# Kernel optimization log

Hardware: AMD Instinct MI355X
Metric: run time of the kernel (lower is better)

## Reference

```python
import jax, jax.numpy as jnp
import numpy as np

HEADS = 16

def setup_inputs() -> dict:
    key = jax.random.key(0)
    k1, k2, k3 = jax.random.split(key, 3)
    B, T, C = 4, 2048, 1024
    s = 0.02
    return {
        "x": jax.random.normal(k1, (B, T, C), dtype=jnp.float32),
        "W_qkv": jax.random.normal(k2, (C, 3 * C), dtype=jnp.float32) * s,
        "b_qkv": jnp.zeros((3 * C,), dtype=jnp.float32),
        "W_pr": jax.random.normal(k3, (C, C), dtype=jnp.float32) * s,
        "b_pr": jnp.zeros((C,), dtype=jnp.float32),
    }

def reference(x, W_qkv, b_qkv, W_pr, b_pr):
    B, T, C = x.shape
    H = HEADS
    hd = C // H
    qkv = x @ W_qkv + b_qkv                     # [B,T,3C]
    q, k, v = jnp.split(qkv, 3, axis=-1)
    # [B,T,C] -> [B,H,T,hd]
    q = q.reshape(B, T, H, hd).transpose(0, 2, 1, 3)
    k = k.reshape(B, T, H, hd).transpose(0, 2, 1, 3)
    v = v.reshape(B, T, H, hd).transpose(0, 2, 1, 3)
    att = jnp.einsum('bhqd,bhkd->bhqk', q, k) * (1.0 / jnp.sqrt(jnp.float32(hd)))
    causal = jnp.tril(jnp.ones((T, T), dtype=bool))
    att = jnp.where(causal[None, None, :, :], att, jnp.float32(-jnp.inf))
    att = jax.nn.softmax(att, axis=-1)
    y = jnp.einsum('bhqk,bhkd->bhqd', att, v)   # [B,H,T,hd]
    y = y.transpose(0, 2, 1, 3).reshape(B, T, C)  # merge heads
    return y @ W_pr + b_pr
```

## Files before the change

kernel.cpp:

```cpp
#include <hip/hip_runtime.h>


typedef __attribute__((ext_vector_type(8))) short bf16x8;
typedef __attribute__((ext_vector_type(4))) float f32x4;

#define MFMA16(a, b, c) __builtin_amdgcn_mfma_f32_16x16x32_bf16(a, b, c, 0, 0, 0)

#define QK_SCALE 0.1803368801111244f

__device__ __forceinline__ unsigned short f2bf(float f) {
    union { float f; unsigned u; } v; v.f = f;
    unsigned r = v.u + 0x7fffu + ((v.u >> 16) & 1u);
    return (unsigned short)(r >> 16);
}

typedef __attribute__((address_space(1))) const unsigned int guint;
typedef __attribute__((address_space(3))) unsigned int luint;
__device__ __forceinline__ void gload16(const void* g, void* l) {
    __builtin_amdgcn_global_load_lds((guint*)g, (luint*)l, 16, 0, 0);
}

__device__ __forceinline__ float exp2_hw(float x) {
    float y;
    asm("v_exp_f32 %0, %1" : "=v"(y) : "v"(x));
    return y;
}

__device__ __forceinline__ unsigned cvt_pk_bf16(float lo, float hi) {
    unsigned w;
    asm("v_cvt_pk_bf16_f32 %0, %1, %2" : "=v"(w) : "v"(lo), "v"(hi));
    return w;
}

__global__ __launch_bounds__(256) void k_conv(const float* __restrict__ in,
                                              unsigned short* __restrict__ out,
                                              int n4) {
    int i = blockIdx.x * 256 + threadIdx.x;
    if (i >= n4) return;
    float4 v = reinterpret_cast<const float4*>(in)[i];
    ushort4 o;
    o.x = f2bf(v.x); o.y = f2bf(v.y); o.z = f2bf(v.z); o.w = f2bf(v.w);
    reinterpret_cast<ushort4*>(out)[i] = o;
}

__global__ __launch_bounds__(256) void k_transpose_conv(const float* __restrict__ W,
                                                        unsigned short* __restrict__ Wt,
                                                        int K, int N) {
    __shared__ unsigned short tile[32][33];
    int tx = threadIdx.x & 31, ty = threadIdx.x >> 5;
    int bn = blockIdx.x * 32, bk = blockIdx.y * 32;
#pragma unroll
    for (int i = 0; i < 32; i += 8)
        tile[ty + i][tx] = f2bf(W[(size_t)(bk + ty + i) * N + bn + tx]);
    __syncthreads();
#pragma unroll
    for (int i = 0; i < 32; i += 8)
        Wt[(size_t)(bn + ty + i) * K + bk + tx] = tile[tx][ty + i];
}

__device__ __forceinline__ int swz_src_col(int off) {
    return ((((off >> 4) & 3) ^ ((off >> 7) & 3)) << 3);
}

__global__ __launch_bounds__(256) void k_gemm_qkv(
    const unsigned short* __restrict__ A,
    const unsigned short* __restrict__ Bt,
    const float* __restrict__ bias,
    unsigned short* __restrict__ Qo,
    unsigned short* __restrict__ Ko,
    unsigned short* __restrict__ Vto)
{
    constexpr int K = 1024;
    __shared__ alignas(16) char smem[33280];
    unsigned short* As = (unsigned short*)smem;
    unsigned short* Bs = (unsigned short*)(smem + 8192);
    unsigned short* Ep = (unsigned short*)smem;
    const int tid = threadIdx.x;
    const int wave = tid >> 6, lane = tid & 63;
    const int wr = wave >> 1, wc = wave & 1;
    const int lrow = lane & 15, lkg = lane >> 4;
    const int bm = blockIdx.y * 128, bn = blockIdx.x * 128;

    const int off0 = tid * 16, off1 = off0 + 4096;
    const unsigned short* gA0 = A + (size_t)(bm + (off0 >> 6)) * K + swz_src_col(off0);
    const unsigned short* gA1 = A + (size_t)(bm + (off1 >> 6)) * K + swz_src_col(off1);
    const unsigned short* gB0 = Bt + (size_t)(bn + (off0 >> 6)) * K + swz_src_col(off0);
    const unsigned short* gB1 = Bt + (size_t)(bn + (off1 >> 6)) * K + swz_src_col(off1);

    f32x4 acc[4][4] = {};

    for (int kt = 0; kt < K; kt += 32) {
        gload16(gA0 + kt, (char*)As + off0);
        gload16(gA1 + kt, (char*)As + off1);
        gload16(gB0 + kt, (char*)Bs + off0);
        gload16(gB1 + kt, (char*)Bs + off1);
        __syncthreads();
        bf16x8 af[4], bfr[4];
#pragma unroll
        for (int m = 0; m < 4; ++m) {
            int R = wr * 64 + m * 16 + lrow;
            af[m] = *reinterpret_cast<const bf16x8*>(
                (const char*)As + R * 64 + ((lkg ^ ((R >> 1) & 3)) << 4));
        }
#pragma unroll
        for (int n = 0; n < 4; ++n) {
            int R = wc * 64 + n * 16 + lrow;
            bfr[n] = *reinterpret_cast<const bf16x8*>(
                (const char*)Bs + R * 64 + ((lkg ^ ((R >> 1) & 3)) << 4));
        }
#pragma unroll
        for (int m = 0; m < 4; ++m)
#pragma unroll
            for (int n = 0; n < 4; ++n)
                acc[m][n] = MFMA16(af[m], bfr[n], acc[m][n]);
        __syncthreads();
    }

    const int which = bn >> 10;
    const int h0 = (bn & 1023) >> 6;
    const int bq = bm >> 11;
    const int t0 = bm & 2047;
    const float qs = (which == 0) ? QK_SCALE : 1.0f;

#pragma unroll
    for (int m = 0; m < 4; ++m) {
        int rl = wr * 64 + m * 16 + lkg * 4;
#pragma unroll
        for (int n = 0; n < 4; ++n) {
            int cl = wc * 64 + n * 16 + lrow;
            float bia = bias[bn + cl];
#pragma unroll
            for (int r = 0; r < 4; ++r) {
                unsigned short val = f2bf((acc[m][n][r] + bia) * qs);
                if (which == 2) {
                    int tl = rl + r;
                    int pt = (tl & 0x60) | ((tl & 15) << 1) | ((tl >> 4) & 1);
                    Ep[cl * 130 + pt] = val;
                } else {
                    Ep[(rl + r) * 130 + cl] = val;
                }
            }
        }
    }
    __syncthreads();

    const int chunk = tid & 15, rbase = tid >> 4;
    if (which != 2) {
        const int head = chunk >> 3, d0 = (chunk & 7) * 8;
        unsigned short* dst = (which == 0 ? Qo : Ko) +
            (size_t)((bq * 16 + h0 + head) * 2048 + t0) * 64 + d0;
#pragma unroll
        for (int s = 0; s < 8; ++s) {
            int row = s * 16 + rbase;
            bf16x8 v = *reinterpret_cast<const bf16x8*>(&Ep[row * 130 + chunk * 8]);
            *reinterpret_cast<bf16x8*>(dst + (size_t)row * 64) = v;
        }
    } else {
#pragma unroll
        for (int s = 0; s < 8; ++s) {
            int pd = s * 16 + rbase;
            bf16x8 v = *reinterpret_cast<const bf16x8*>(&Ep[pd * 130 + chunk * 8]);
            int bh = bq * 16 + h0 + (pd >> 6);
            size_t addr = ((size_t)(bh * 64 + (pd & 63)) * 2048) + t0 + chunk * 8;
            *reinterpret_cast<bf16x8*>(Vto + addr) = v;
        }
    }
}

__global__ __launch_bounds__(256, 2) void k_attn(
    const unsigned short* __restrict__ Q,
    const unsigned short* __restrict__ Kg,
    const unsigned short* __restrict__ Vt,
    unsigned short* __restrict__ Y)
{
    __shared__ alignas(16) unsigned short Ks[2][4096];
    __shared__ alignas(16) unsigned short Vs[2][4096];
    __shared__ unsigned int Pu[4][32][36];
    const int tid = threadIdx.x;
    const int wave = tid >> 6, lane = tid & 63;
    const int lrow = lane & 15, lkg = lane >> 4;
    const int bh = blockIdx.x & 63;
    const int s = (blockIdx.x >> 6) & 3;
    const int band = blockIdx.x >> 8;
    const int j = (band == 0) ? 15 - s : (band == 1) ? 8 + s : (band == 2) ? 7 - s : s;
    const int qt = 4 * j + wave;
    const int q0 = qt * 32;
    const int nt = 2 * j + 2;
    const int b = bh >> 4, hh = bh & 15;

    const unsigned short* Qh = Q + (size_t)bh * 2048 * 64;
    const unsigned short* Kh = Kg + (size_t)bh * 2048 * 64;
    const unsigned short* Vh = Vt + (size_t)bh * 64 * 2048;

    const int srow = tid >> 3;
    const int swz = ((tid & 7) ^ (srow & 7)) << 3;
    const unsigned short* gK = Kh + (size_t)srow * 64 + swz;
    const unsigned short* gV = Vh + (size_t)srow * 2048 + swz;
    char* dK0 = (char*)&Ks[0][0] + tid * 16;
    char* dV0 = (char*)&Vs[0][0] + tid * 16;

    bf16x8 aq[2][2];
#pragma unroll
    for (int h = 0; h < 2; ++h)
#pragma unroll
        for (int ks = 0; ks < 2; ++ks)
            aq[h][ks] = *reinterpret_cast<const bf16x8*>(
                &Qh[(size_t)(q0 + h * 16 + lrow) * 64 + ks * 32 + lkg * 8]);

    f32x4 acc[2][4] = {};
    float lsum[2][4] = {};

#define STAGE(kb_, bufn_)                                           \
    do {                                                            \
        const unsigned short* k0_ = gK + (kb_) * 64;                \
        const unsigned short* v0_ = gV + (kb_);                     \
        char* dk_ = dK0 + (bufn_) * 8192;                           \
        char* dv_ = dV0 + (bufn_) * 8192;                           \
        gload16(k0_, dk_);                                          \
        gload16(k0_ + 2048, dk_ + 4096);                            \
        gload16(v0_, dv_);                                          \
        gload16(v0_ + 65536, dv_ + 4096);                           \
    } while (0)

    STAGE(0, 0);
    int buf = 0;

    for (int t = 0; t < nt; ++t) {
        if (t + 1 < nt) {
            STAGE((t + 1) * 64, buf ^ 1);
            asm volatile("s_waitcnt vmcnt(4)" ::: "memory");
        } else {
            asm volatile("s_waitcnt vmcnt(0)" ::: "memory");
        }
        __builtin_amdgcn_s_barrier();
        __builtin_amdgcn_sched_barrier(0);

        const int kb = t * 64;
        const char* kbase = (const char*)&Ks[buf][0];
        const char* vbase = (const char*)&Vs[buf][0];

        f32x4 s_[2][4] = {};
        __builtin_amdgcn_s_setprio(1);
#pragma unroll
        for (int sub = 0; sub < 4; ++sub) {
            int krow = sub * 16 + lrow;
            bf16x8 kf0 = *reinterpret_cast<const bf16x8*>(
                kbase + krow * 128 + ((lkg ^ (krow & 7)) << 4));
            bf16x8 kf1 = *reinterpret_cast<const bf16x8*>(
                kbase + krow * 128 + (((4 + lkg) ^ (krow & 7)) << 4));
            s_[0][sub] = MFMA16(aq[0][0], kf0, s_[0][sub]);
            s_[0][sub] = MFMA16(aq[0][1], kf1, s_[0][sub]);
            s_[1][sub] = MFMA16(aq[1][0], kf0, s_[1][sub]);
            s_[1][sub] = MFMA16(aq[1][1], kf1, s_[1][sub]);
        }
        __builtin_amdgcn_s_setprio(0);

        const bool need_mask = (kb + 64 > q0);
#pragma unroll
        for (int h = 0; h < 2; ++h)
#pragma unroll
            for (int sub = 0; sub < 4; ++sub)
#pragma unroll
                for (int r = 0; r < 4; ++r) {
                    float v = s_[h][sub][r];
                    if (need_mask) {
                        int key = kb + sub * 16 + lrow;
                        int q = q0 + h * 16 + lkg * 4 + r;
                        v = (key <= q) ? v : -1e30f;
                    }
                    s_[h][sub][r] = exp2_hw(v);
                }

#pragma unroll
        for (int h = 0; h < 2; ++h) {
            int prow = h * 16 + lkg * 4;
#pragma unroll
            for (int r = 0; r < 4; ++r) {
                lsum[h][r] += (s_[h][0][r] + s_[h][1][r]) + (s_[h][2][r] + s_[h][3][r]);
                Pu[wave][prow + r][lrow]      = cvt_pk_bf16(s_[h][0][r], s_[h][1][r]);
                Pu[wave][prow + r][16 + lrow] = cvt_pk_bf16(s_[h][2][r], s_[h][3][r]);
            }
        }

        bf16x8 pf[2][2];
#pragma unroll
        for (int h = 0; h < 2; ++h)
#pragma unroll
            for (int kc = 0; kc < 2; ++kc)
                pf[h][kc] = *reinterpret_cast<const bf16x8*>(
                    &Pu[wave][h * 16 + lrow][kc * 16 + lkg * 4]);

        __builtin_amdgcn_s_setprio(1);
#pragma unroll
        for (int tt = 0; tt < 4; ++tt) {
            int vrow = tt * 16 + lrow;
            bf16x8 vf0 = *reinterpret_cast<const bf16x8*>(
                vbase + vrow * 128 + ((lkg ^ (vrow & 7)) << 4));
            bf16x8 vf1 = *reinterpret_cast<const bf16x8*>(
                vbase + vrow * 128 + (((4 + lkg) ^ (vrow & 7)) << 4));
            acc[0][tt] = MFMA16(pf[0][0], vf0, acc[0][tt]);
            acc[0][tt] = MFMA16(pf[0][1], vf1, acc[0][tt]);
            acc[1][tt] = MFMA16(pf[1][0], vf0, acc[1][tt]);
            acc[1][tt] = MFMA16(pf[1][1], vf1, acc[1][tt]);
        }
        __builtin_amdgcn_s_setprio(0);

        __builtin_amdgcn_s_barrier();
        buf ^= 1;
    }
#undef STAGE

#pragma unroll
    for (int h = 0; h < 2; ++h) {
        float inv[4];
#pragma unroll
        for (int r = 0; r < 4; ++r) {
            float l = lsum[h][r];
            l += __shfl_xor(l, 1); l += __shfl_xor(l, 2);
            l += __shfl_xor(l, 4); l += __shfl_xor(l, 8);
            inv[r] = 1.0f / l;
        }
#pragma unroll
        for (int t = 0; t < 4; ++t)
#pragma unroll
            for (int r = 0; r < 4; ++r) {
                int q = q0 + h * 16 + lkg * 4 + r;
                size_t idx = ((size_t)b * 2048 + q) * 1024 + hh * 64 + t * 16 + lrow;
                Y[idx] = f2bf(acc[h][t][r] * inv[r]);
            }
    }
}

__global__ __launch_bounds__(256) void k_gemm_proj(
    const unsigned short* __restrict__ A,
    const unsigned short* __restrict__ Bt,
    const float* __restrict__ bias,
    float* __restrict__ out)
{
    constexpr int K = 1024;
    __shared__ alignas(16) char smem[33024];
    unsigned short* As = (unsigned short*)smem;
    unsigned short* Bs = (unsigned short*)(smem + 8192);
    float* Ep2 = (float*)smem;
    const int tid = threadIdx.x;
    const int wave = tid >> 6, lane = tid & 63;
    const int wr = wave >> 1, wc = wave & 1;
    const int lrow = lane & 15, lkg = lane >> 4;
    const int bm = blockIdx.y * 128, bn = blockIdx.x * 128;

    const int off0 = tid * 16, off1 = off0 + 4096;
    const unsigned short* gA0 = A + (size_t)(bm + (off0 >> 6)) * K + swz_src_col(off0);
    const unsigned short* gA1 = A + (size_t)(bm + (off1 >> 6)) * K + swz_src_col(off1);
    const unsigned short* gB0 = Bt + (size_t)(bn + (off0 >> 6)) * K + swz_src_col(off0);
    const unsigned short* gB1 = Bt + (size_t)(bn + (off1 >> 6)) * K + swz_src_col(off1);

    f32x4 acc[4][4] = {};

    for (int kt = 0; kt < K; kt += 32) {
        gload16(gA0 + kt, (char*)As + off0);
        gload16(gA1 + kt, (char*)As + off1);
        gload16(gB0 + kt, (char*)Bs + off0);
        gload16(gB1 + kt, (char*)Bs + off1);
        __syncthreads();
        bf16x8 af[4], bfr[4];
#pragma unroll
        for (int m = 0; m < 4; ++m) {
            int R = wr * 64 + m * 16 + lrow;
            af[m] = *reinterpret_cast<const bf16x8*>(
                (const char*)As + R * 64 + ((lkg ^ ((R >> 1) & 3)) << 4));
        }
#pragma unroll
        for (int n = 0; n < 4; ++n) {
            int R = wc * 64 + n * 16 + lrow;
            bfr[n] = *reinterpret_cast<const bf16x8*>(
                (const char*)Bs + R * 64 + ((lkg ^ ((R >> 1) & 3)) << 4));
        }
#pragma unroll
        for (int m = 0; m < 4; ++m)
#pragma unroll
            for (int n = 0; n < 4; ++n)
                acc[m][n] = MFMA16(af[m], bfr[n], acc[m][n]);
        __syncthreads();
    }

    const int chunk = tid >> 3;
    const int r8 = tid & 7;
#pragma unroll
    for (int p = 0; p < 2; ++p) {
        if (p) __syncthreads();
        if (wr == p) {
#pragma unroll
            for (int m = 0; m < 4; ++m)
#pragma unroll
                for (int n = 0; n < 4; ++n) {
                    int cl = wc * 64 + n * 16 + lrow;
                    float bia = bias[bn + cl];
#pragma unroll
                    for (int r = 0; r < 4; ++r)
                        Ep2[(m * 16 + lkg * 4 + r) * 129 + cl] = acc[m][n][r] + bia;
                }
        }
        __syncthreads();
#pragma unroll
        for (int s = 0; s < 8; ++s) {
            int row = r8 * 8 + s;
            float4 v = *reinterpret_cast<const float4*>(&Ep2[row * 129 + chunk * 4]);
            *reinterpret_cast<float4*>(&out[(size_t)(bm + p * 64 + row) * 1024 + bn + chunk * 4]) = v;
        }
    }
}

extern "C" void kernel_launch(void* const* d_in, const int* in_sizes, int n_in,
                              void* d_out, int out_size, void* d_ws, size_t ws_size,
                              hipStream_t stream) {
    const float* x    = (const float*)d_in[0];
    const float* Wqkv = (const float*)d_in[1];
    const float* bqkv = (const float*)d_in[2];
    const float* Wpr  = (const float*)d_in[3];
    const float* bpr  = (const float*)d_in[4];
    float* out = (float*)d_out;

    char* ws = (char*)d_ws;
    unsigned short* xb  = (unsigned short*)(ws);
    unsigned short* Wqt = (unsigned short*)(ws + 16777216);
    unsigned short* Wpt = (unsigned short*)(ws + 23068672);
    unsigned short* Qb  = (unsigned short*)(ws + 25165824);
    unsigned short* Kb  = (unsigned short*)(ws + 41943040);
    unsigned short* Vt  = (unsigned short*)(ws + 58720256);
    unsigned short* Y   = xb;

    k_conv<<<8192, 256, 0, stream>>>(x, xb, 8388608 / 4);
    k_transpose_conv<<<dim3(96, 32), 256, 0, stream>>>(Wqkv, Wqt, 1024, 3072);
    k_transpose_conv<<<dim3(32, 32), 256, 0, stream>>>(Wpr, Wpt, 1024, 1024);
    k_gemm_qkv<<<dim3(24, 64), 256, 0, stream>>>(xb, Wqt, bqkv, Qb, Kb, Vt);
    k_attn<<<1024, 256, 0, stream>>>(Qb, Kb, Vt, Y);
    k_gemm_proj<<<dim3(8, 64), 256, 0, stream>>>(Y, Wpt, bpr, out);
}
```

Before: 184.1 us.

## Double-buffer LDS tiles in QKV and projection GEMMs with prefetch

Both GEMM kernels now load the next K-tile into a second LDS buffer while the current tile is consumed. They wait only on the older loads with explicit vmcnt counts and raw s_barrier, and raise wave priority around the MFMA block. This is meant to hide global-to-LDS load latency that previously stalled each iteration behind a full __syncthreads. The cost is double the staging LDS, 32KB of the existing 33KB allocation. Correctness depends on the hand-written waitcnt and barrier ordering, including the added sync before the projection epilogue reuses smem.

```diff
diff --git a/kernel.cpp b/kernel.cpp
--- a/kernel.cpp
+++ b/kernel.cpp
@@ -72,8 +72,6 @@
 {
     constexpr int K = 1024;
     __shared__ alignas(16) char smem[33280];
-    unsigned short* As = (unsigned short*)smem;
-    unsigned short* Bs = (unsigned short*)(smem + 8192);
     unsigned short* Ep = (unsigned short*)smem;
     const int tid = threadIdx.x;
     const int wave = tid >> 6, lane = tid & 63;
@@ -89,32 +87,53 @@
 
     f32x4 acc[4][4] = {};
 
-    for (int kt = 0; kt < K; kt += 32) {
-        gload16(gA0 + kt, (char*)As + off0);
-        gload16(gA1 + kt, (char*)As + off1);
-        gload16(gB0 + kt, (char*)Bs + off0);
-        gload16(gB1 + kt, (char*)Bs + off1);
-        __syncthreads();
+#define GSTAGE(kt_, bufn_)                                          \
+    do {                                                            \
+        char* ba_ = smem + (bufn_) * 16384;                         \
+        gload16(gA0 + (kt_), ba_ + off0);                           \
+        gload16(gA1 + (kt_), ba_ + off1);                           \
+        gload16(gB0 + (kt_), ba_ + 8192 + off0);                    \
+        gload16(gB1 + (kt_), ba_ + 8192 + off1);                    \
+    } while (0)
+
+    GSTAGE(0, 0);
+    int buf = 0;
+    for (int t = 0; t < 32; ++t) {
+        if (t < 31) {
+            GSTAGE((t + 1) * 32, buf ^ 1);
+            asm volatile("s_waitcnt vmcnt(4)" ::: "memory");
+        } else {
+            asm volatile("s_waitcnt vmcnt(0)" ::: "memory");
+        }
+        __builtin_amdgcn_s_barrier();
+        __builtin_amdgcn_sched_barrier(0);
+
+        const char* Asb = smem + buf * 16384;
+        const char* Bsb = Asb + 8192;
         bf16x8 af[4], bfr[4];
 #pragma unroll
         for (int m = 0; m < 4; ++m) {
             int R = wr * 64 + m * 16 + lrow;
             af[m] = *reinterpret_cast<const bf16x8*>(
-                (const char*)As + R * 64 + ((lkg ^ ((R >> 1) & 3)) << 4));
+                Asb + R * 64 + ((lkg ^ ((R >> 1) & 3)) << 4));
         }
 #pragma unroll
         for (int n = 0; n < 4; ++n) {
             int R = wc * 64 + n * 16 + lrow;
             bfr[n] = *reinterpret_cast<const bf16x8*>(
-                (const char*)Bs + R * 64 + ((lkg ^ ((R >> 1) & 3)) << 4));
-        }
+                Bsb + R * 64 + ((lkg ^ ((R >> 1) & 3)) << 4));
+        }
+        __builtin_amdgcn_s_setprio(1);
 #pragma unroll
         for (int m = 0; m < 4; ++m)
 #pragma unroll
             for (int n = 0; n < 4; ++n)
                 acc[m][n] = MFMA16(af[m], bfr[n], acc[m][n]);
-        __syncthreads();
-    }
+        __builtin_amdgcn_s_setprio(0);
+        __builtin_amdgcn_s_barrier();
+        buf ^= 1;
+    }
+#undef GSTAGE
 
     const int which = bn >> 10;
     const int h0 = (bn & 1023) >> 6;
@@ -339,8 +358,6 @@
 {
     constexpr int K = 1024;
     __shared__ alignas(16) char smem[33024];
-    unsigned short* As = (unsigned short*)smem;
-    unsigned short* Bs = (unsigned short*)(smem + 8192);
     float* Ep2 = (float*)smem;
     const int tid = threadIdx.x;
     const int wave = tid >> 6, lane = tid & 63;
@@ -356,38 +373,59 @@
 
     f32x4 acc[4][4] = {};
 
-    for (int kt = 0; kt < K; kt += 32) {
-        gload16(gA0 + kt, (char*)As + off0);
-        gload16(gA1 + kt, (char*)As + off1);
-        gload16(gB0 + kt, (char*)Bs + off0);
-        gload16(gB1 + kt, (char*)Bs + off1);
-        __syncthreads();
+#define GSTAGE(kt_, bufn_)                                          \
+    do {                                                            \
+        char* ba_ = smem + (bufn_) * 16384;                         \
+        gload16(gA0 + (kt_), ba_ + off0);                           \
+        gload16(gA1 + (kt_), ba_ + off1);                           \
+        gload16(gB0 + (kt_), ba_ + 8192 + off0);                    \
+        gload16(gB1 + (kt_), ba_ + 8192 + off1);                    \
+    } while (0)
+
+    GSTAGE(0, 0);
+    int buf = 0;
+    for (int t = 0; t < 32; ++t) {
+        if (t < 31) {
+            GSTAGE((t + 1) * 32, buf ^ 1);
+            asm volatile("s_waitcnt vmcnt(4)" ::: "memory");
+        } else {
+            asm volatile("s_waitcnt vmcnt(0)" ::: "memory");
+        }
+        __builtin_amdgcn_s_barrier();
+        __builtin_amdgcn_sched_barrier(0);
+
+        const char* Asb = smem + buf * 16384;
+        const char* Bsb = Asb + 8192;
         bf16x8 af[4], bfr[4];
 #pragma unroll
         for (int m = 0; m < 4; ++m) {
             int R = wr * 64 + m * 16 + lrow;
             af[m] = *reinterpret_cast<const bf16x8*>(
-                (const char*)As + R * 64 + ((lkg ^ ((R >> 1) & 3)) << 4));
+                Asb + R * 64 + ((lkg ^ ((R >> 1) & 3)) << 4));
         }
 #pragma unroll
         for (int n = 0; n < 4; ++n) {
             int R = wc * 64 + n * 16 + lrow;
             bfr[n] = *reinterpret_cast<const bf16x8*>(
-                (const char*)Bs + R * 64 + ((lkg ^ ((R >> 1) & 3)) << 4));
-        }
+                Bsb + R * 64 + ((lkg ^ ((R >> 1) & 3)) << 4));
+        }
+        __builtin_amdgcn_s_setprio(1);
 #pragma unroll
         for (int m = 0; m < 4; ++m)
 #pragma unroll
             for (int n = 0; n < 4; ++n)
                 acc[m][n] = MFMA16(af[m], bfr[n], acc[m][n]);
-        __syncthreads();
-    }
+        __builtin_amdgcn_s_setprio(0);
+        __builtin_amdgcn_s_barrier();
+        buf ^= 1;
+    }
+#undef GSTAGE
 
     const int chunk = tid >> 3;
     const int r8 = tid & 7;
 #pragma unroll
     for (int p = 0; p < 2; ++p) {
-        if (p) __syncthreads();
+        __syncthreads();
         if (wr == p) {
 #pragma unroll
             for (int m = 0; m < 4; ++m)
```

New measurement: 178.4 us. -3.1%, faster.
